# Kernel optimization log

Hardware: AMD Instinct MI355X
Metric: run time of the kernel (lower is better)

Reference implementation:

```python
import jax, jax.numpy as jnp
import numpy as np

DIM, NHEADS, HEAD_DIM = 1536, 12, 128
EPS = 1e-6
ROPE_SPLIT = (22, 21, 21)  # head_dim//2 = 64 -> (c-2*(c//3), c//3, c//3)


def setup_inputs() -> dict:
    key = jax.random.key(0)
    ks = jax.random.split(key, 12)
    B, F, H, W = 1, 8, 16, 28
    L = F * H * W  # 3584
    inp = {
        "x": jax.random.normal(ks[0], (B, L, DIM), jnp.float32),
        "seq_lens": jnp.full((B,), L, dtype=jnp.int64),
        "grid_sizes": jnp.array([[F, H, W]] * B, dtype=jnp.int64),
        "freqs": jax.random.uniform(ks[1], (1024, HEAD_DIM // 2), jnp.float32) * (2 * np.pi),
        "Wq": jax.random.normal(ks[2], (DIM, DIM), jnp.float32) / np.sqrt(DIM),
        "bq": jnp.zeros((DIM,), jnp.float32),
        "Wk": jax.random.normal(ks[3], (DIM, DIM), jnp.float32) / np.sqrt(DIM),
        "bk": jnp.zeros((DIM,), jnp.float32),
        "Wv": jax.random.normal(ks[4], (DIM, DIM), jnp.float32) / np.sqrt(DIM),
        "bv": jnp.zeros((DIM,), jnp.float32),
        "Wo": jax.random.normal(ks[5], (DIM, DIM), jnp.float32) / np.sqrt(DIM),
        "bo": jnp.zeros((DIM,), jnp.float32),
        "gq": jnp.ones((DIM,), jnp.float32),
        "gk": jnp.ones((DIM,), jnp.float32),
    }
    return inp


def _rms_norm(x, g):
    var = jnp.mean(jnp.square(x), axis=-1, keepdims=True)
    return x * jax.lax.rsqrt(var + EPS) * g


def _rope_angles(freqs, F, H, W):
    # freqs: [1024, 64] angles; split per 3D axis and broadcast over the grid
    cf, ch, cw = ROPE_SPLIT
    af = freqs[:F, :cf]
    ah = freqs[:H, cf:cf + ch]
    aw = freqs[:W, cf + ch:]
    ang = jnp.concatenate([
        jnp.broadcast_to(af[:, None, None, :], (F, H, W, cf)),
        jnp.broadcast_to(ah[None, :, None, :], (F, H, W, ch)),
        jnp.broadcast_to(aw[None, None, :, :], (F, H, W, cw)),
    ], axis=-1).reshape(F * H * W, cf + ch + cw)  # [L, 64]
    return jnp.cos(ang), jnp.sin(ang)


def _rope_apply(x, cos, sin):
    # x: [B, L, N, D]; complex multiply by unit-modulus freqs, in real arithmetic
    b, s, n, d = x.shape
    xr = x.reshape(b, s, n, d // 2, 2)
    a, bi = xr[..., 0], xr[..., 1]
    c = cos[None, :, None, :]
    si = sin[None, :, None, :]
    out = jnp.stack([a * c - bi * si, a * si + bi * c], axis=-1)
    return out.reshape(b, s, n, d)


def reference(x, seq_lens, grid_sizes, freqs, Wq, bq, Wk, bk, Wv, bv, Wo, bo, gq, gk):
    b, s, _ = x.shape
    n, d = NHEADS, HEAD_DIM
    gs = np.asarray(grid_sizes)
    F, H, W = int(gs[0, 0]), int(gs[0, 1]), int(gs[0, 2])  # static grid (same per batch)

    q = _rms_norm(x @ Wq + bq, gq).reshape(b, s, n, d)
    k = _rms_norm(x @ Wk + bk, gk).reshape(b, s, n, d)
    v = (x @ Wv + bv).reshape(b, s, n, d)

    cos, sin = _rope_angles(freqs, F, H, W)
    q = _rope_apply(q, cos, sin)
    k = _rope_apply(k, cos, sin)

    # full attention with key-length masking (flash_attention k_lens semantics)
    scale = 1.0 / np.sqrt(d)
    scores = jnp.einsum("bqnd,bknd->bnqk", q, k) * scale
    key_mask = jnp.arange(s)[None, :] < seq_lens[:, None]  # [B, S]
    scores = jnp.where(key_mask[:, None, None, :], scores, -1e9)
    probs = jax.nn.softmax(scores, axis=-1)
    out = jnp.einsum("bnqk,bknd->bqnd", probs, v)

    return out.reshape(b, s, n * d) @ Wo + bo
```

## Files before the change

kernel.cpp:

```cpp
#include <hip/hip_runtime.h>

typedef __bf16 bf16;
typedef __bf16 bf16x8 __attribute__((ext_vector_type(8)));
typedef __bf16 bf16x4 __attribute__((ext_vector_type(4)));
typedef float f32x4 __attribute__((ext_vector_type(4)));

__device__ __forceinline__ void gload_lds16(const void* g, void* l) {
  __builtin_amdgcn_global_load_lds(
      (const __attribute__((address_space(1))) void*)g,
      (__attribute__((address_space(3))) void*)l, 16, 0, 0);
}

__device__ __forceinline__ bf16x8 ld8(const bf16* p) {
  bf16x8 v; __builtin_memcpy(&v, p, 16); return v;
}

__global__ __launch_bounds__(256) void cast_f32_bf16(const float* __restrict__ in,
                                                     bf16* __restrict__ out, int n8) {
  int i = blockIdx.x * 256 + threadIdx.x;
  if (i >= n8) return;
  const float4* p = (const float4*)in + (size_t)i * 2;
  float4 a = p[0], b = p[1];
  bf16x8 o;
  o[0] = (bf16)a.x; o[1] = (bf16)a.y; o[2] = (bf16)a.z; o[3] = (bf16)a.w;
  o[4] = (bf16)b.x; o[5] = (bf16)b.y; o[6] = (bf16)b.z; o[7] = (bf16)b.w;
  *((bf16x8*)out + i) = o;
}

__global__ __launch_bounds__(256) void transpose_w(const float* __restrict__ W,
                                                   bf16* __restrict__ Wt) {
  __shared__ bf16 tile[64][72];
  int t = threadIdx.x;
  int k0 = blockIdx.x * 64, n0 = blockIdx.y * 64;
  int r = t >> 2, c0 = (t & 3) * 16;
  const float* src = W + (size_t)(k0 + r) * 1536 + n0 + c0;
#pragma unroll
  for (int q = 0; q < 4; ++q) {
    float4 v = *(const float4*)(src + q * 4);
    tile[c0 + q * 4 + 0][r] = (bf16)v.x;
    tile[c0 + q * 4 + 1][r] = (bf16)v.y;
    tile[c0 + q * 4 + 2][r] = (bf16)v.z;
    tile[c0 + q * 4 + 3][r] = (bf16)v.w;
  }
  __syncthreads();
  bf16* dst = Wt + (size_t)(n0 + r) * 1536 + k0 + c0;
  bf16x8 o0, o1;
#pragma unroll
  for (int j = 0; j < 8; ++j) { o0[j] = tile[r][c0 + j]; o1[j] = tile[r][c0 + 8 + j]; }
  *(bf16x8*)dst = o0;
  *(bf16x8*)(dst + 8) = o1;
}

__global__ void concat_bias(const float* __restrict__ bq, const float* __restrict__ bk,
                            const float* __restrict__ bv, float* __restrict__ o) {
  int t = blockIdx.x * 256 + threadIdx.x;
  if (t < 1536) o[t] = bq[t];
  else if (t < 3072) o[t] = bk[t - 1536];
  else if (t < 4608) o[t] = bv[t - 3072];
}

template <typename OUT>
__global__ __launch_bounds__(256, 2) void gemm_bt(const bf16* __restrict__ A, const bf16* __restrict__ B,
                                                  const float* __restrict__ bias, OUT* __restrict__ C,
                                                  int M, int N, int K) {
  __shared__ bf16 As[128 * 32], Bs[128 * 32];
  int t = threadIdx.x, l = t & 63, w = t >> 6;
  int lane15 = l & 15, lhi = l >> 4;
  int m0 = blockIdx.x * 128, n0 = blockIdx.y * 128;
  int wm = (w >> 1) * 64, wn = (w & 1) * 64;
  f32x4 zero = {0.f, 0.f, 0.f, 0.f};
  f32x4 acc[4][4];
#pragma unroll
  for (int i = 0; i < 4; ++i)
#pragma unroll
    for (int j = 0; j < 4; ++j) acc[i][j] = zero;

  int srow = t >> 2, scol = (t & 3) * 8;
  const bf16* gA0 = A + (size_t)(m0 + srow) * K + scol;
  const bf16* gA1 = A + (size_t)(m0 + 64 + srow) * K + scol;
  const bf16* gB0 = B + (size_t)(n0 + srow) * K + scol;
  const bf16* gB1 = B + (size_t)(n0 + 64 + srow) * K + scol;
  char* ldsA = (char*)As + (size_t)w * 1024;
  char* ldsB = (char*)Bs + (size_t)w * 1024;

  for (int kt = 0; kt < K; kt += 32) {
    gload_lds16(gA0 + kt, ldsA);
    gload_lds16(gA1 + kt, ldsA + 4096);
    gload_lds16(gB0 + kt, ldsB);
    gload_lds16(gB1 + kt, ldsB + 4096);
    __syncthreads();
    bf16x8 af[4], bfr[4];
#pragma unroll
    for (int i = 0; i < 4; ++i) {
      af[i]  = ld8(&As[(wm + i * 16 + lane15) * 32 + lhi * 8]);
      bfr[i] = ld8(&Bs[(wn + i * 16 + lane15) * 32 + lhi * 8]);
    }
#pragma unroll
    for (int i = 0; i < 4; ++i)
#pragma unroll
      for (int j = 0; j < 4; ++j)
        acc[i][j] = __builtin_amdgcn_mfma_f32_16x16x32_bf16(af[i], bfr[j], acc[i][j], 0, 0, 0);
    __syncthreads();
  }
#pragma unroll
  for (int i = 0; i < 4; ++i)
#pragma unroll
    for (int j = 0; j < 4; ++j) {
      int col = n0 + wn + j * 16 + lane15;
      float bb = bias[col];
#pragma unroll
      for (int r = 0; r < 4; ++r) {
        int row = m0 + wm + i * 16 + lhi * 4 + r;
        C[(size_t)row * N + col] = (OUT)(acc[i][j][r] + bb);
      }
    }
}

__global__ void rope_tab(const float* __restrict__ freqs, const int* __restrict__ gs,
                         float* __restrict__ tabc, float* __restrict__ tabs) {
  int idx = blockIdx.x * 256 + threadIdx.x;
  if (idx >= 3584 * 64) return;
  int s = idx >> 6, i = idx & 63;
  int H = gs[1], W = gs[2];
  int f = s / (H * W);
  int rem = s - f * (H * W);
  int hh = rem / W;
  int ww = rem - hh * W;
  int row = (i < 22) ? f : ((i < 43) ? hh : ww);
  float a = freqs[row * 64 + i];
  tabc[idx] = cosf(a);
  tabs[idx] = sinf(a);
}

__global__ __launch_bounds__(256) void postproc(const bf16* __restrict__ QKV,
    const float* __restrict__ gq, const float* __restrict__ gk,
    const float* __restrict__ tabc, const float* __restrict__ tabs,
    bf16* __restrict__ qb, bf16* __restrict__ kb) {
  int s = blockIdx.x, t = threadIdx.x;
  const bf16* Qr = QKV + (size_t)s * 4608;
  const bf16* Kr = Qr + 1536;
  int j0 = t * 6;
  float qv[6], kv[6];
  float sq = 0.f, sk = 0.f;
#pragma unroll
  for (int j = 0; j < 6; ++j) {
    float a = (float)Qr[j0 + j]; qv[j] = a; sq += a * a;
    float b = (float)Kr[j0 + j]; kv[j] = b; sk += b * b;
  }
#pragma unroll
  for (int off = 32; off > 0; off >>= 1) {
    sq += __shfl_down(sq, off);
    sk += __shfl_down(sk, off);
  }
  __shared__ float red[2][4];
  if ((t & 63) == 0) { red[0][t >> 6] = sq; red[1][t >> 6] = sk; }
  __syncthreads();
  float vq = (red[0][0] + red[0][1]) + (red[0][2] + red[0][3]);
  float vk = (red[1][0] + red[1][1]) + (red[1][2] + red[1][3]);
  float rq = 1.0f / sqrtf(vq * (1.0f / 1536.0f) + 1e-6f);
  float rk = 1.0f / sqrtf(vk * (1.0f / 1536.0f) + 1e-6f);
  rq *= 0.08838834764831845f;
#pragma unroll
  for (int j = 0; j < 6; j += 2) {
    int jj = j0 + j;
    int d = jj & 127, i = d >> 1, h = jj >> 7;
    float c = tabc[s * 64 + i], sn = tabs[s * 64 + i];
    size_t qbase = (((size_t)h * 3584 + s) << 7) + d;
    float a = qv[j] * rq * gq[jj], b = qv[j + 1] * rq * gq[jj + 1];
    qb[qbase] = (bf16)(a * c - b * sn);
    qb[qbase + 1] = (bf16)(a * sn + b * c);
    size_t kbase = (((size_t)(h * 56 + (s >> 6)) * 64 + (s & 63)) << 7) + (d ^ ((s & 7) << 3));
    float ak = kv[j] * rk * gk[jj], bk2 = kv[j + 1] * rk * gk[jj + 1];
    kb[kbase] = (bf16)(ak * c - bk2 * sn);
    kb[kbase + 1] = (bf16)(ak * sn + bk2 * c);
  }
}

__global__ __launch_bounds__(256) void transpose_v(const bf16* __restrict__ QKV,
                                                   bf16* __restrict__ vT) {
  __shared__ bf16 tile[128][72];
  int t = threadIdx.x;
  int h = blockIdx.y;
  int s0 = blockIdx.x * 64;
  int r = t >> 2, c0 = (t & 3) * 32;
  const bf16* src = QKV + (size_t)(s0 + r) * 4608 + 3072 + h * 128 + c0;
#pragma unroll
  for (int q = 0; q < 4; ++q) {
    bf16x8 v = ld8(src + q * 8);
#pragma unroll
    for (int j = 0; j < 8; ++j) tile[c0 + q * 8 + j][r] = v[j];
  }
  __syncthreads();
  int d = t >> 1, spHalf = t & 1;
  int sw = (d & 7) << 3;
  bf16* dstBase = vT + ((size_t)(h * 56 + blockIdx.x) * 128 + d) * 64;
#pragma unroll
  for (int q = 0; q < 4; ++q) {
    int mm = spHalf * 4 + q;
    int sA = 32 * (mm >> 2) + 16 * (mm & 1) + 4 * ((mm >> 1) & 1);
    bf16x4 lo, hi;
#pragma unroll
    for (int j = 0; j < 4; ++j) {
      lo[j] = tile[d][spHalf * 32 + q * 8 + j];
      hi[j] = tile[d][spHalf * 32 + q * 8 + 4 + j];
    }
    int slo = sA ^ sw;
    *(bf16x4*)(dstBase + slo) = lo;
    *(bf16x4*)(dstBase + (slo ^ 8)) = hi;
  }
}

__global__ __launch_bounds__(256, 2) void flash_attn(
    const bf16* __restrict__ qb, const bf16* __restrict__ kb, const bf16* __restrict__ vT,
    const int* __restrict__ sl, bf16* __restrict__ po0, bf16* __restrict__ po1,
    bf16* __restrict__ po2, bf16* __restrict__ po3, float* __restrict__ ml) {
  const int L = 3584;
  __shared__ bf16 Ks[64 * 128];
  __shared__ bf16 Vs[128 * 64];
  int t = threadIdx.x, l = t & 63, w = t >> 6;
  int lane15 = l & 15, lhi = l >> 4;
  int grp48 = l & 48;
  int b = blockIdx.x;
  int xcd = b & 7, k_ = b >> 3;
  int pg = k_ / 28, x = k_ - pg * 28;
  int p = pg * 8 + xcd;
  int h = p % 12, z = p / 12;
  int qw = x * 128 + w * 32;
  int seqlen = sl[0];
  bf16* po = (z == 0) ? po0 : (z == 1) ? po1 : (z == 2) ? po2 : po3;
  float* mlz = ml + (size_t)z * 12 * L * 2;

  bf16x8 aq[2][4];
#pragma unroll
  for (int qf = 0; qf < 2; ++qf)
#pragma unroll
    for (int kc = 0; kc < 4; ++kc)
      aq[qf][kc] = ld8(qb + (((size_t)h * L + qw + qf * 16 + lane15) << 7) + kc * 32 + lhi * 8);

  f32x4 zero = {0.f, 0.f, 0.f, 0.f};
  f32x4 out[2][8];
  float m2[2] = {-1e30f, -1e30f}, ls2[2] = {0.f, 0.f};
#pragma unroll
  for (int qf = 0; qf < 2; ++qf)
#pragma unroll
    for (int df = 0; df < 8; ++df) out[qf][df] = zero;

  int nt = (seqlen + 63) >> 6;
  if (nt > 56) nt = 56;
  int t0 = z * 14, t1 = t0 + 14;
  if (t0 > nt) t0 = nt;
  if (t1 > nt) t1 = nt;

  int src_off = w * 1024 + l * 16;
  char* ksd = (char*)Ks + w * 1024;
  char* vsd = (char*)Vs + w * 1024;

  for (int ti = t0; ti < t1; ++ti) {
    int kv0 = ti * 64;
    __syncthreads();
    {
      const char* kimg = (const char*)kb + ((size_t)(h * 56) + ti) * 16384;
      const char* vimg = (const char*)vT + ((size_t)(h * 56) + ti) * 16384;
#pragma unroll
      for (int pp = 0; pp < 4; ++pp) {
        gload_lds16(kimg + pp * 4096 + src_off, ksd + pp * 4096);
        gload_lds16(vimg + pp * 4096 + src_off, vsd + pp * 4096);
      }
    }
    __syncthreads();

    f32x4 sc[2][4];
#pragma unroll
    for (int qf = 0; qf < 2; ++qf)
#pragma unroll
      for (int a = 0; a < 4; ++a) sc[qf][a] = zero;
#pragma unroll
    for (int a = 0; a < 4; ++a) {
      int rk = a * 16 + lane15;
      const char* krow = (const char*)Ks + rk * 256;
      int swz = (rk & 7) << 4;
#pragma unroll
      for (int kc = 0; kc < 4; ++kc) {
        bf16x8 bk_ = ld8((const bf16*)(krow + ((kc * 64 + lhi * 16) ^ swz)));
        sc[0][a] = __builtin_amdgcn_mfma_f32_16x16x32_bf16(bk_, aq[0][kc], sc[0][a], 0, 0, 0);
        sc[1][a] = __builtin_amdgcn_mfma_f32_16x16x32_bf16(bk_, aq[1][kc], sc[1][a], 0, 0, 0);
      }
    }

    bool full = (kv0 + 64 <= seqlen);
    bf16x8 ap[2][2];
#pragma unroll
    for (int qf = 0; qf < 2; ++qf) {
      float tm = -1e30f;
#pragma unroll
      for (int a = 0; a < 4; ++a)
#pragma unroll
        for (int r = 0; r < 4; ++r) {
          float s = sc[qf][a][r];
          if (!full) {
            int col = kv0 + a * 16 + lhi * 4 + r;
            s = (col < seqlen) ? s : -1e30f;
            sc[qf][a][r] = s;
          }
          tm = fmaxf(tm, s);
        }
      tm = fmaxf(tm, __shfl_xor(tm, 16));
      tm = fmaxf(tm, __shfl_xor(tm, 32));
      if (!__all(tm <= m2[qf] + 8.0f)) {
        float nm = fmaxf(m2[qf], tm);
        float f = __expf(m2[qf] - nm);
        m2[qf] = nm;
        ls2[qf] *= f;
#pragma unroll
        for (int r = 0; r < 4; ++r) {
          float fr = __shfl(f, grp48 | (lhi * 4 + r));
#pragma unroll
          for (int df = 0; df < 8; ++df) out[qf][df][r] *= fr;
        }
      }
      float psum = 0.f;
#pragma unroll
      for (int a = 0; a < 4; ++a)
#pragma unroll
        for (int r = 0; r < 4; ++r) {
          float pv = __expf(sc[qf][a][r] - m2[qf]);
          sc[qf][a][r] = pv;
          psum += pv;
        }
      psum += __shfl_xor(psum, 16);
      psum += __shfl_xor(psum, 32);
      ls2[qf] += psum;
#pragma unroll
      for (int c = 0; c < 2; ++c) {
        bf16x8 f8;
#pragma unroll
        for (int r = 0; r < 4; ++r) {
          f8[r] = (bf16)sc[qf][2 * c][r];
          f8[r + 4] = (bf16)sc[qf][2 * c + 1][r];
        }
        ap[qf][c] = f8;
      }
    }

#pragma unroll
    for (int df = 0; df < 8; ++df) {
      int rd = df * 16 + lane15;
      const char* vrow2 = (const char*)Vs + rd * 128;
      int swz = (rd & 7) << 4;
#pragma unroll
      for (int c = 0; c < 2; ++c) {
        bf16x8 bv_ = ld8((const bf16*)(vrow2 + ((c * 64 + lhi * 16) ^ swz)));
        out[0][df] = __builtin_amdgcn_mfma_f32_16x16x32_bf16(ap[0][c], bv_, out[0][df], 0, 0, 0);
        out[1][df] = __builtin_amdgcn_mfma_f32_16x16x32_bf16(ap[1][c], bv_, out[1][df], 0, 0, 0);
      }
    }
  }

#pragma unroll
  for (int qf = 0; qf < 2; ++qf) {
#pragma unroll
    for (int r = 0; r < 4; ++r) {
      int row = qw + qf * 16 + lhi * 4 + r;
      size_t rbase = ((size_t)h * L + row) << 7;
#pragma unroll
      for (int df = 0; df < 8; ++df)
        po[rbase + df * 16 + lane15] = (bf16)out[qf][df][r];
    }
    if (lhi == 0) {
      int row = qw + qf * 16 + lane15;
      mlz[(((size_t)h * L + row) << 1)] = m2[qf];
      mlz[(((size_t)h * L + row) << 1) + 1] = ls2[qf];
    }
  }
}

__global__ __launch_bounds__(256) void combine4(
    const bf16* __restrict__ po0, const bf16* __restrict__ po1,
    const bf16* __restrict__ po2, const bf16* __restrict__ po3,
    const float* __restrict__ ml, bf16* __restrict__ attn) {
  const int L = 3584;
  int row = blockIdx.x * 8 + (threadIdx.x >> 5);
  int c0 = (threadIdx.x & 31) * 4;
  const size_t mls = (size_t)12 * L * 2;
  float m0 = ml[row * 2],           l0 = ml[row * 2 + 1];
  float m1 = ml[mls + row * 2],     l1 = ml[mls + row * 2 + 1];
  float m2 = ml[2 * mls + row * 2], l2 = ml[2 * mls + row * 2 + 1];
  float m3 = ml[3 * mls + row * 2], l3 = ml[3 * mls + row * 2 + 1];
  float M = fmaxf(fmaxf(m0, m1), fmaxf(m2, m3));
  float w0 = __expf(m0 - M), w1 = __expf(m1 - M);
  float w2 = __expf(m2 - M), w3 = __expf(m3 - M);
  float inv = 1.0f / fmaxf(w0 * l0 + w1 * l1 + w2 * l2 + w3 * l3, 1e-30f);
  bf16x4 a, b, c, d;
  __builtin_memcpy(&a, po0 + (size_t)row * 128 + c0, 8);
  __builtin_memcpy(&b, po1 + (size_t)row * 128 + c0, 8);
  __builtin_memcpy(&c, po2 + (size_t)row * 128 + c0, 8);
  __builtin_memcpy(&d, po3 + (size_t)row * 128 + c0, 8);
  int h = row / L, s = row % L;
  bf16x4 o;
#pragma unroll
  for (int j = 0; j < 4; ++j)
    o[j] = (bf16)((w0 * (float)a[j] + w1 * (float)b[j] + w2 * (float)c[j] + w3 * (float)d[j]) * inv);
  *(bf16x4*)(attn + (size_t)s * 1536 + h * 128 + c0) = o;
}

extern "C" void kernel_launch(void* const* d_in, const int* in_sizes, int n_in,
                              void* d_out, int out_size, void* d_ws, size_t ws_size,
                              hipStream_t stream) {
  const float* x = (const float*)d_in[0];
  const int* seq_lens = (const int*)d_in[1];
  const int* grid_sizes = (const int*)d_in[2];
  const float* freqs = (const float*)d_in[3];
  const float* Wq = (const float*)d_in[4];
  const float* bq = (const float*)d_in[5];
  const float* Wk = (const float*)d_in[6];
  const float* bk = (const float*)d_in[7];
  const float* Wv = (const float*)d_in[8];
  const float* bv = (const float*)d_in[9];
  const float* Wo = (const float*)d_in[10];
  const float* bo = (const float*)d_in[11];
  const float* gq = (const float*)d_in[12];
  const float* gk = (const float*)d_in[13];

  char* ws = (char*)d_ws;
  bf16* x_bf = (bf16*)(ws + 0);
  bf16* wqkvt = (bf16*)(ws + 11010048);
  bf16* wot = (bf16*)(ws + 25165824);
  float* bqkv = (float*)(ws + 29884416);
  bf16* QKV = (bf16*)(ws + 29902848);
  bf16* qb = (bf16*)(ws + 62932992);
  bf16* kb = (bf16*)(ws + 73943040);
  bf16* vT = (bf16*)(ws + 84953088);
  float* tabc = (float*)(ws + 95963136);
  float* tabs = (float*)(ws + 96880640);
  bf16* po0 = (bf16*)(ws + 29902848);
  bf16* attn = (bf16*)(ws + 51922944);
  bf16* po1 = (bf16*)(ws + 0);
  bf16* po2 = (bf16*)(ws + 11010048);
  float* ml  = (float*)(ws + 95963136);
  bf16* po3 = (bf16*)(ws + 97798144);

  cast_f32_bf16<<<2688, 256, 0, stream>>>(x, x_bf, 688128);
  transpose_w<<<dim3(24, 24), 256, 0, stream>>>(Wq, wqkvt);
  transpose_w<<<dim3(24, 24), 256, 0, stream>>>(Wk, wqkvt + 1536 * 1536);
  transpose_w<<<dim3(24, 24), 256, 0, stream>>>(Wv, wqkvt + 2 * 1536 * 1536);
  transpose_w<<<dim3(24, 24), 256, 0, stream>>>(Wo, wot);
  concat_bias<<<18, 256, 0, stream>>>(bq, bk, bv, bqkv);
  rope_tab<<<896, 256, 0, stream>>>(freqs, grid_sizes, tabc, tabs);
  gemm_bt<bf16><<<dim3(28, 36), 256, 0, stream>>>(x_bf, wqkvt, bqkv, QKV, 3584, 4608, 1536);
  postproc<<<3584, 256, 0, stream>>>(QKV, gq, gk, tabc, tabs, qb, kb);
  transpose_v<<<dim3(56, 12), 256, 0, stream>>>(QKV, vT);
  flash_attn<<<1344, 256, 0, stream>>>(qb, kb, vT, seq_lens, po0, po1, po2, po3, ml);
  combine4<<<5376, 256, 0, stream>>>(po0, po1, po2, po3, ml, attn);
  gemm_bt<float><<<dim3(28, 12), 256, 0, stream>>>(attn, wot, bo, (float*)d_out, 3584, 1536, 1536);
}
```

Before: 274.8 us.

## Double-buffer K/V tiles in LDS and switch softmax to exp2

The flash attention loop now keeps two LDS buffers for K and V. It prefetches the next tile with global_load_lds while the current tile runs through the MFMAs, so there is one barrier per iteration instead of two. The 1/ln2 factor is folded into the query scale, which lets softmax and the combine kernel use exp2f instead of __expf, with the rescale threshold adjusted to match. The cost is twice the LDS per block (64KB), which may limit occupancy. The compiler may also insert conservative vmcnt waits that cancel the overlap.

```diff
diff --git a/kernel.cpp b/kernel.cpp
--- a/kernel.cpp
+++ b/kernel.cpp
@@ -159,7 +159,7 @@
   float vk = (red[1][0] + red[1][1]) + (red[1][2] + red[1][3]);
   float rq = 1.0f / sqrtf(vq * (1.0f / 1536.0f) + 1e-6f);
   float rk = 1.0f / sqrtf(vk * (1.0f / 1536.0f) + 1e-6f);
-  rq *= 0.08838834764831845f;
+  rq *= 0.08838834764831845f * 1.44269504088896340f;
 #pragma unroll
   for (int j = 0; j < 6; j += 2) {
     int jj = j0 + j;
@@ -215,8 +215,8 @@
     const int* __restrict__ sl, bf16* __restrict__ po0, bf16* __restrict__ po1,
     bf16* __restrict__ po2, bf16* __restrict__ po3, float* __restrict__ ml) {
   const int L = 3584;
-  __shared__ bf16 Ks[64 * 128];
-  __shared__ bf16 Vs[128 * 64];
+  __shared__ bf16 Ks[2][64 * 128];
+  __shared__ bf16 Vs[2][128 * 64];
   int t = threadIdx.x, l = t & 63, w = t >> 6;
   int lane15 = l & 15, lhi = l >> 4;
   int grp48 = l & 48;
@@ -252,22 +252,35 @@
   if (t1 > nt) t1 = nt;
 
   int src_off = w * 1024 + l * 16;
-  char* ksd = (char*)Ks + w * 1024;
-  char* vsd = (char*)Vs + w * 1024;
-
+
+  if (t0 < t1) {
+    const char* kimg = (const char*)kb + ((size_t)(h * 56) + t0) * 16384;
+    const char* vimg = (const char*)vT + ((size_t)(h * 56) + t0) * 16384;
+#pragma unroll
+    for (int pp = 0; pp < 4; ++pp) {
+      gload_lds16(kimg + pp * 4096 + src_off, (char*)Ks[0] + w * 1024 + pp * 4096);
+      gload_lds16(vimg + pp * 4096 + src_off, (char*)Vs[0] + w * 1024 + pp * 4096);
+    }
+  }
+
+  int cur = 0;
   for (int ti = t0; ti < t1; ++ti) {
     int kv0 = ti * 64;
     __syncthreads();
-    {
-      const char* kimg = (const char*)kb + ((size_t)(h * 56) + ti) * 16384;
-      const char* vimg = (const char*)vT + ((size_t)(h * 56) + ti) * 16384;
+    if (ti + 1 < t1) {
+      const char* kimg = (const char*)kb + ((size_t)(h * 56) + ti + 1) * 16384;
+      const char* vimg = (const char*)vT + ((size_t)(h * 56) + ti + 1) * 16384;
+      char* ksd = (char*)Ks[cur ^ 1] + w * 1024;
+      char* vsd = (char*)Vs[cur ^ 1] + w * 1024;
 #pragma unroll
       for (int pp = 0; pp < 4; ++pp) {
         gload_lds16(kimg + pp * 4096 + src_off, ksd + pp * 4096);
         gload_lds16(vimg + pp * 4096 + src_off, vsd + pp * 4096);
       }
     }
-    __syncthreads();
+
+    const char* Kc = (const char*)Ks[cur];
+    const char* Vc = (const char*)Vs[cur];
 
     f32x4 sc[2][4];
 #pragma unroll
@@ -277,7 +290,7 @@
 #pragma unroll
     for (int a = 0; a < 4; ++a) {
       int rk = a * 16 + lane15;
-      const char* krow = (const char*)Ks + rk * 256;
+      const char* krow = Kc + rk * 256;
       int swz = (rk & 7) << 4;
 #pragma unroll
       for (int kc = 0; kc < 4; ++kc) {
@@ -306,9 +319,9 @@
         }
       tm = fmaxf(tm, __shfl_xor(tm, 16));
       tm = fmaxf(tm, __shfl_xor(tm, 32));
-      if (!__all(tm <= m2[qf] + 8.0f)) {
+      if (!__all(tm <= m2[qf] + 11.5416f)) {
         float nm = fmaxf(m2[qf], tm);
-        float f = __expf(m2[qf] - nm);
+        float f = exp2f(m2[qf] - nm);
         m2[qf] = nm;
         ls2[qf] *= f;
 #pragma unroll
@@ -323,7 +336,7 @@
       for (int a = 0; a < 4; ++a)
 #pragma unroll
         for (int r = 0; r < 4; ++r) {
-          float pv = __expf(sc[qf][a][r] - m2[qf]);
+          float pv = exp2f(sc[qf][a][r] - m2[qf]);
           sc[qf][a][r] = pv;
           psum += pv;
         }
@@ -345,7 +358,7 @@
 #pragma unroll
     for (int df = 0; df < 8; ++df) {
       int rd = df * 16 + lane15;
-      const char* vrow2 = (const char*)Vs + rd * 128;
+      const char* vrow2 = Vc + rd * 128;
       int swz = (rd & 7) << 4;
 #pragma unroll
       for (int c = 0; c < 2; ++c) {
@@ -354,6 +367,7 @@
         out[1][df] = __builtin_amdgcn_mfma_f32_16x16x32_bf16(ap[1][c], bv_, out[1][df], 0, 0, 0);
       }
     }
+    cur ^= 1;
   }
 
 #pragma unroll
@@ -387,8 +401,8 @@
   float m2 = ml[2 * mls + row * 2], l2 = ml[2 * mls + row * 2 + 1];
   float m3 = ml[3 * mls + row * 2], l3 = ml[3 * mls + row * 2 + 1];
   float M = fmaxf(fmaxf(m0, m1), fmaxf(m2, m3));
-  float w0 = __expf(m0 - M), w1 = __expf(m1 - M);
-  float w2 = __expf(m2 - M), w3 = __expf(m3 - M);
+  float w0 = exp2f(m0 - M), w1 = exp2f(m1 - M);
+  float w2 = exp2f(m2 - M), w3 = exp2f(m3 - M);
   float inv = 1.0f / fmaxf(w0 * l0 + w1 * l1 + w2 * l2 + w3 * l3, 1e-30f);
   bf16x4 a, b, c, d;
   __builtin_memcpy(&a, po0 + (size_t)row * 128 + c0, 8);
```

Result: slower. 292.9 us (+6.6%).
